# Optimization experiments

Measured on AMD Instinct MI355X. Metric: run time of the kernel, lower is better.

Reference implementation:

```python
import jax, jax.numpy as jnp
import numpy as np

DN = ('NCHW', 'OIHW', 'NCHW')
BN_EPS = 1e-5


def _conv3x3(x, w, b):
    y = jax.lax.conv_general_dilated(x, w, (1, 1), ((1, 1), (1, 1)), dimension_numbers=DN)
    return y + b[None, :, None, None]


def _bn(x, g, b, m, v):
    # eval-mode BatchNorm with running stats
    scale = g * jax.lax.rsqrt(v + BN_EPS)
    return (x - m[None, :, None, None]) * scale[None, :, None, None] + b[None, :, None, None]


def _bilinear_gather(x, py, px):
    # x: [B,C,H,W]; py, px: [B,K,H,W] float sampling coords (zero padding outside)
    B, C, H, W = x.shape
    y0 = jnp.floor(py)
    x0 = jnp.floor(px)
    wy = py - y0
    wx = px - x0
    y0i = y0.astype(jnp.int32)
    x0i = x0.astype(jnp.int32)
    xf = x.reshape(B, C, H * W)

    def corner(yi, xi, wgt):
        valid = (yi >= 0) & (yi < H) & (xi >= 0) & (xi < W)
        idx = jnp.clip(yi, 0, H - 1) * W + jnp.clip(xi, 0, W - 1)  # [B,K,H,W]
        g = jax.vmap(lambda xb, ib: xb[:, ib])(xf, idx)            # [B,C,K,H,W]
        return g * (wgt * valid.astype(x.dtype))[:, None]

    v = corner(y0i, x0i, (1 - wy) * (1 - wx))
    v = v + corner(y0i, x0i + 1, (1 - wy) * wx)
    v = v + corner(y0i + 1, x0i, wy * (1 - wx))
    v = v + corner(y0i + 1, x0i + 1, wy * wx)
    return v  # [B,C,K,H,W]


def _deform_conv(x, offset, mask, w):
    # modulated deformable conv: 3x3, stride 1, pad 1, dilation 1, groups=1, dg=1
    B, C, H, W = x.shape
    K = 9
    ky = jnp.arange(K) // 3 - 1  # kernel row offsets
    kx = jnp.arange(K) % 3 - 1   # kernel col offsets
    dy = offset[:, :K]           # [B,K,H,W]
    dx = offset[:, K:]
    py = dy + (ky[:, None, None] + jnp.arange(H)[None, :, None]).astype(x.dtype)
    px = dx + (kx[:, None, None] + jnp.arange(W)[None, None, :]).astype(x.dtype)
    val = _bilinear_gather(x, py, px) * mask[:, None]  # [B,C,K,H,W]
    O = w.shape[0]
    return jnp.einsum('bckhw,ock->bohw', val, w.reshape(O, C, K))


def _deconv(x, w):
    # ConvTranspose2d k=4 s=2 p=1, bias=False; torch weight layout [Cin, Cout, 4, 4]
    wk = jnp.flip(w, (2, 3)).transpose(1, 0, 2, 3)  # [Cout, Cin, 4, 4]
    return jax.lax.conv_general_dilated(x, wk, (1, 1), ((2, 2), (2, 2)),
                                        lhs_dilation=(2, 2), dimension_numbers=DN)


def setup_inputs() -> dict:
    key = jax.random.key(0)
    ks = jax.random.split(key, 14)
    B, Cin, Cout, H, W = 8, 256, 256, 64, 64
    x = jax.random.normal(ks[0], (B, Cin, H, W), jnp.float32)
    w_off = jax.random.normal(ks[1], (27, Cin, 3, 3), jnp.float32) * 0.01
    b_off = jnp.zeros((27,), jnp.float32)
    w_dcn = jax.random.normal(ks[2], (Cout, Cin, 3, 3), jnp.float32) * (2.0 / (Cin * 9)) ** 0.5
    gamma1 = 1.0 + 0.1 * jax.random.normal(ks[3], (Cout,), jnp.float32)
    beta1 = 0.1 * jax.random.normal(ks[4], (Cout,), jnp.float32)
    mean1 = 0.1 * jax.random.normal(ks[5], (Cout,), jnp.float32)
    var1 = jax.random.uniform(ks[6], (Cout,), jnp.float32, 0.5, 1.5)
    w_up = jax.random.normal(ks[7], (Cout, Cout, 4, 4), jnp.float32) * 0.05
    gamma2 = 1.0 + 0.1 * jax.random.normal(ks[8], (Cout,), jnp.float32)
    beta2 = 0.1 * jax.random.normal(ks[9], (Cout,), jnp.float32)
    mean2 = 0.1 * jax.random.normal(ks[10], (Cout,), jnp.float32)
    var2 = jax.random.uniform(ks[11], (Cout,), jnp.float32, 0.5, 1.5)
    return dict(x=x, w_off=w_off, b_off=b_off, w_dcn=w_dcn,
                gamma1=gamma1, beta1=beta1, mean1=mean1, var1=var1,
                w_up=w_up, gamma2=gamma2, beta2=beta2, mean2=mean2, var2=var2)


def reference(x, w_off, b_off, w_dcn, gamma1, beta1, mean1, var1,
              w_up, gamma2, beta2, mean2, var2):
    offset_mask = _conv3x3(x, w_off, b_off)          # [B,27,H,W]
    ox, oy, m = jnp.split(offset_mask, 3, axis=1)
    offset = jnp.concatenate([ox, oy], axis=1)       # [B,18,H,W]
    mask = jax.nn.sigmoid(m)                         # [B,9,H,W]
    y = _deform_conv(x, offset, mask, w_dcn)
    y = jax.nn.relu(_bn(y, gamma1, beta1, mean1, var1))
    up = _deconv(y, w_up)
    up = jax.nn.relu(_bn(up, gamma2, beta2, mean2, var2))
    return (y, up)
```

## Files before the change

kernel.cpp:

```cpp
#include <hip/hip_runtime.h>
#include <cstddef>


#define B_EPS 1e-5f

typedef __bf16 bf16x8 __attribute__((ext_vector_type(8)));
typedef float f32x4 __attribute__((ext_vector_type(4)));
typedef unsigned short u16;
typedef unsigned int u32;

__device__ __forceinline__ u32 bfr(float f) {
    u32 u = __float_as_uint(f);
    return (u + 0x7FFFu + ((u >> 16) & 1u)) >> 16;
}

__device__ __forceinline__ void gather8(const float* cb2, uint4 q, int g8, f32x4* ga) {
    const float* p00 = cb2 + ((size_t)(q.x & 0xFFFFu) << 5) + g8;
    const float* p01 = cb2 + ((size_t)(q.x >> 16) << 5) + g8;
    const float* p10 = cb2 + ((size_t)(q.y & 0xFFFFu) << 5) + g8;
    const float* p11 = cb2 + ((size_t)(q.y >> 16) << 5) + g8;
    ga[0] = *(const f32x4*)p00; ga[1] = *(const f32x4*)(p00 + 4);
    ga[2] = *(const f32x4*)p01; ga[3] = *(const f32x4*)(p01 + 4);
    ga[4] = *(const f32x4*)p10; ga[5] = *(const f32x4*)(p10 + 4);
    ga[6] = *(const f32x4*)p11; ga[7] = *(const f32x4*)(p11 + 4);
}

__device__ __forceinline__ uint4 packv(uint4 q, const f32x4* ga) {
    const float w00 = __uint_as_float(q.z << 16);
    const float w01 = __uint_as_float(q.z & 0xFFFF0000u);
    const float w10 = __uint_as_float(q.w << 16);
    const float w11 = __uint_as_float(q.w & 0xFFFF0000u);
    union { bf16x8 h; uint4 u; } r;
#pragma unroll
    for (int jj = 0; jj < 4; ++jj) {
        r.h[jj]     = (__bf16)fmaf(w00, ga[0][jj], fmaf(w01, ga[2][jj], fmaf(w10, ga[4][jj], w11 * ga[6][jj])));
        r.h[4 + jj] = (__bf16)fmaf(w00, ga[1][jj], fmaf(w01, ga[3][jj], fmaf(w10, ga[5][jj], w11 * ga[7][jj])));
    }
    return r.u;
}

__global__ __launch_bounds__(256) void k_tr_woff(const float* __restrict__ w,
                                                 float* __restrict__ o) {
    int i = blockIdx.x * 256 + threadIdx.x;
    int t9 = i % 9; int r = i / 9; int c = r & 255; int co = r >> 8;
    o[c * 243 + co * 9 + t9] = w[i];
}

__global__ __launch_bounds__(256) void k_prep_wdb(const float* __restrict__ w,
                                                  u16* __restrict__ o) {
    int i = blockIdx.x * 256 + threadIdx.x;
    int kk = i & 31; int e = i >> 5;
    int oc = e & 255; int ch = e >> 8;
    int cc = ch & 7; int k = ch >> 3;
    o[i] = (u16)bfr(w[oc * 2304 + (cc * 32 + kk) * 9 + k]);
}

__global__ __launch_bounds__(256) void k_prep_wtb(const float* __restrict__ w,
                                                  u16* __restrict__ o) {
    int i = blockIdx.x * 256 + threadIdx.x;
    int kk = i & 31; int e = i >> 5;
    int oc = e & 255; e >>= 8;
    int cc = e & 31; int cls = e >> 5;
    int tap = kk >> 3, ci = cc * 8 + (kk & 7);
    int ca = cls >> 1, cb = cls & 1;
    int wr = (tap >> 1) ? (ca ? 0 : 1) : (ca ? 2 : 3);
    int wc = (tap & 1) ? (cb ? 0 : 1) : (cb ? 2 : 3);
    o[i] = (u16)bfr(w[ci * 4096 + oc * 16 + wr * 4 + wc]);
}

__global__ __launch_bounds__(256) void k_bn_prep(
    const float* g1, const float* be1, const float* mu1, const float* va1,
    const float* g2, const float* be2, const float* mu2, const float* va2,
    float* bnp) {
    int t = threadIdx.x;
    float s1 = g1[t] * rsqrtf(va1[t] + B_EPS);
    bnp[t] = s1; bnp[256 + t] = be1[t] - mu1[t] * s1;
    float s2 = g2[t] * rsqrtf(va2[t] + B_EPS);
    bnp[512 + t] = s2; bnp[768 + t] = be2[t] - mu2[t] * s2;
}

__global__ __launch_bounds__(256) void k_om_init(const float* __restrict__ b_off,
                                                 float* __restrict__ om) {
    int i = blockIdx.x * 256 + threadIdx.x;
    int co = (i >> 12) % 27;
    om[i] = b_off[co];
}

__global__ __launch_bounds__(256) void k_tr_x(const float* __restrict__ x,
                                              float* __restrict__ xt) {
    const int t = threadIdx.x;
    const int pg = blockIdx.x & 15;
    const int cc = (blockIdx.x >> 4) & 7;
    const int b = blockIdx.x >> 7;
    const int pix = (pg << 8) + t;
    const float* xp = x + ((size_t)b << 20) + ((size_t)(cc << 5) << 12) + pix;
    float v[32];
#pragma unroll
    for (int cl = 0; cl < 32; ++cl) v[cl] = xp[(size_t)cl << 12];
    float* op = xt + ((size_t)b << 20) + ((size_t)cc << 17) + ((size_t)pix << 5);
#pragma unroll
    for (int i = 0; i < 8; ++i)
        *(f32x4*)(op + i * 4) = *(const f32x4*)&v[i * 4];
}

__global__ __launch_bounds__(256) void k_tr_y(const float* __restrict__ y,
                                              u16* __restrict__ yt) {
    const int t = threadIdx.x;
    const int blk = blockIdx.x % 18;
    const int oc = (blockIdx.x / 18) & 7;
    const int b = blockIdx.x / 144;
    const int hp = blk * 256 + t;
    if (hp >= 4356) return;
    const int h = hp / 66, w = hp % 66;
    u16* dstb = yt + (((size_t)b * 32 + oc * 4) * 4356 + hp) * 8;
    if (h == 0 || h == 65 || w == 0 || w == 65) {
        uint4 z = make_uint4(0, 0, 0, 0);
#pragma unroll
        for (int j = 0; j < 4; ++j)
            *(uint4*)(dstb + (size_t)j * (4356 * 8)) = z;
        return;
    }
    const float* yp = y + ((size_t)b << 20) + ((size_t)(oc * 32) << 12)
                    + ((h - 1) << 6) + (w - 1);
    u16 vv[32];
#pragma unroll
    for (int cl = 0; cl < 32; ++cl) vv[cl] = (u16)bfr(yp[(size_t)cl << 12]);
#pragma unroll
    for (int j = 0; j < 4; ++j)
        *(uint4*)(dstb + (size_t)j * (4356 * 8)) = *(const uint4*)&vv[j * 8];
}

__global__ __launch_bounds__(256) void k_offset_conv_part(
    const float* __restrict__ x, const float* __restrict__ wofft,
    float* __restrict__ om)
{
    const int t = threadIdx.x;
    const int chunk = blockIdx.x & 7;
    const int rg = (blockIdx.x >> 3) & 15;
    const int b = blockIdx.x >> 7;
    const int h = (rg << 2) + (t >> 6);
    const int w = t & 63;
    const int c0 = chunk << 5;
    const float* xb = x + ((size_t)b << 20);
    float acc[27];
#pragma unroll
    for (int i = 0; i < 27; ++i) acc[i] = 0.f;
    for (int cl = 0; cl < 32; ++cl) {
        const int c = c0 + cl;
        const float* xc = xb + (c << 12);
        float xv[9];
#pragma unroll
        for (int tr = 0; tr < 3; ++tr) {
            int hh = h + tr - 1;
            bool vy = (unsigned)hh < 64u;
#pragma unroll
            for (int tc = 0; tc < 3; ++tc) {
                int ww = w + tc - 1;
                xv[tr * 3 + tc] = (vy && (unsigned)ww < 64u) ? xc[(hh << 6) + ww] : 0.f;
            }
        }
        const float* wc = wofft + c * 243;
#pragma unroll
        for (int co = 0; co < 27; ++co)
#pragma unroll
            for (int k = 0; k < 9; ++k)
                acc[co] = fmaf(xv[k], wc[co * 9 + k], acc[co]);
    }
    float* omb = om + (size_t)b * 110592 + (h << 6) + w;
#pragma unroll
    for (int co = 0; co < 27; ++co)
        atomicAdd(&omb[co << 12], acc[co]);
}

__global__ __launch_bounds__(256) void k_prep_coeff(
    const float* __restrict__ om, uint4* __restrict__ cpk)
{
    int i = blockIdx.x * 256 + threadIdx.x;
    int pix = i & 4095;
    int bk = i >> 12;
    int k = bk % 9;
    int b = bk / 9;
    int h = pix >> 6, w = pix & 63;
    const float* omb = om + (size_t)b * 110592;
    float dy = omb[(k << 12) + pix];
    float dx = omb[((9 + k) << 12) + pix];
    float mr = omb[((18 + k) << 12) + pix];
    float m  = 1.f / (1.f + __expf(-mr));
    float py = dy + (float)(k / 3 - 1 + h);
    float px = dx + (float)(k % 3 - 1 + w);
    float y0f = floorf(py), x0f = floorf(px);
    float wy = py - y0f, wx = px - x0f;
    int y0 = (int)y0f, x0 = (int)x0f;
    int y1 = y0 + 1, x1 = x0 + 1;
    float vy0 = ((unsigned)y0 < 64u) ? 1.f : 0.f;
    float vy1 = ((unsigned)y1 < 64u) ? 1.f : 0.f;
    float vx0 = ((unsigned)x0 < 64u) ? 1.f : 0.f;
    float vx1 = ((unsigned)x1 < 64u) ? 1.f : 0.f;
    int cy0 = min(max(y0, 0), 63), cy1 = min(max(y1, 0), 63);
    int cx0 = min(max(x0, 0), 63), cx1 = min(max(x1, 0), 63);
    u32 xw = (u32)((cy0 << 6) + cx0) | ((u32)((cy0 << 6) + cx1) << 16);
    u32 yw = (u32)((cy1 << 6) + cx0) | ((u32)((cy1 << 6) + cx1) << 16);
    float w00 = m * (1.f - wy) * (1.f - wx) * vy0 * vx0;
    float w01 = m * (1.f - wy) * wx         * vy0 * vx1;
    float w10 = m * wy         * (1.f - wx) * vy1 * vx0;
    float w11 = m * wy         * wx         * vy1 * vx1;
    u32 zw = bfr(w00) | (bfr(w01) << 16);
    u32 ww2 = bfr(w10) | (bfr(w11) << 16);
    cpk[i] = make_uint4(xw, yw, zw, ww2);
}

__global__ __launch_bounds__(256, 2) void k_deform_mfma(
    const float* __restrict__ xt, const u16* __restrict__ Wdb,
    const uint4* __restrict__ cpk, const float* __restrict__ bnp,
    float* __restrict__ yout)
{
    __shared__ __align__(16) u16 sB[2][64 * 40];
    const int t = threadIdx.x;
    const int row = blockIdx.x & 63;
    const int b = blockIdx.x >> 6;
    const int pix0 = row << 6;
    const int p = t >> 2;
    const int g = t & 3;
    const int g8 = g << 3;
    const float* xtb = xt + ((size_t)b << 20);

    const int lane = t & 63;
    const int wv = t >> 6;
    const int quad = lane >> 4;
    const int ln = lane & 15;
    const u16* Wrow = Wdb + (size_t)(wv * 64 + ln) * 32 + quad * 8;

    f32x4 acc[4][4];
#pragma unroll
    for (int i = 0; i < 4; ++i)
#pragma unroll
        for (int j = 0; j < 4; ++j) acc[i][j] = (f32x4)0.f;

    bf16x8 afb[2][4];
    uint4 qcur = cpk[(size_t)(b * 9) * 4096 + pix0 + p];
    {
#pragma unroll
        for (int mi = 0; mi < 4; ++mi)
            afb[0][mi] = *(const bf16x8*)(Wrow + mi * 512);
        f32x4 ga[8];
        gather8(xtb, qcur, g8, ga);
        *(uint4*)&sB[0][p * 40 + g8] = packv(qcur, ga);
        __syncthreads();
    }

    for (int k = 0; k < 9; ++k) {
        uint4 qnext = qcur;
        if (k < 8) qnext = cpk[(size_t)(b * 9 + k + 1) * 4096 + pix0 + p];
#pragma unroll
        for (int cc = 0; cc < 8; ++cc) {
            const int ch = k * 8 + cc;
            const int par = cc & 1;
            const bool pre = ch < 71;
            const uint4 q = (cc == 7) ? qnext : qcur;
            f32x4 ga[8];
            if (pre) {
                const u16* Wn = Wrow + (size_t)(ch + 1) * 8192;
#pragma unroll
                for (int mi = 0; mi < 4; ++mi)
                    afb[par ^ 1][mi] = *(const bf16x8*)(Wn + mi * 512);
                gather8(xtb + ((size_t)((cc + 1) & 7) << 17), q, g8, ga);
            }
            bf16x8 bg[4];
#pragma unroll
            for (int i = 0; i < 4; ++i)
                bg[i] = *(const bf16x8*)&sB[par][(i * 16 + ln) * 40 + quad * 8];
#pragma unroll
            for (int mi = 0; mi < 4; ++mi)
#pragma unroll
                for (int ni = 0; ni < 4; ++ni)
                    acc[mi][ni] = __builtin_amdgcn_mfma_f32_16x16x32_bf16(
                        afb[par][mi], bg[ni], acc[mi][ni], 0, 0, 0);
            if (pre)
                *(uint4*)&sB[par ^ 1][p * 40 + g8] = packv(q, ga);
            __syncthreads();
        }
        qcur = qnext;
    }

    const float* sc1 = bnp;
    const float* bi1 = bnp + 256;
    float* yb2 = yout + ((size_t)b << 20);
#pragma unroll
    for (int mi = 0; mi < 4; ++mi) {
#pragma unroll
        for (int r = 0; r < 4; ++r) {
            int o = wv * 64 + mi * 16 + quad * 4 + r;
            float sc = sc1[o], bi = bi1[o];
#pragma unroll
            for (int ni = 0; ni < 4; ++ni) {
                float v = fmaxf(fmaf(acc[mi][ni][r], sc, bi), 0.f);
                yb2[((size_t)o << 12) + pix0 + ni * 16 + ln] = v;
            }
        }
    }
}

__global__ __launch_bounds__(256, 4) void k_deconv_mfma(
    const u16* __restrict__ yt, const u16* __restrict__ Wtb,
    const float* __restrict__ bnp, float* __restrict__ up)
{
    const int t = threadIdx.x;
    const int h0 = blockIdx.x & 63;
    const int cls = (blockIdx.x >> 6) & 3;
    const int b = blockIdx.x >> 8;
    const int ca = cls >> 1, cb = cls & 1;
    const int DH0 = ca ? 0 : -1, DH1 = ca ? 1 : 0;
    const int DW0 = cb ? 0 : -1, DW1 = cb ? 1 : 0;

    const int lane = t & 63;
    const int wv = t >> 6;
    const int quad = lane >> 4;
    const int ln = lane & 15;

    const int DHq = (quad >> 1) ? DH1 : DH0;
    const int DWq = (quad & 1) ? DW1 : DW0;

    const u16* ytb = yt + (size_t)b * (32u * 4356 * 8);
    const u16* Bb[4];
#pragma unroll
    for (int i = 0; i < 4; ++i) {
        int pix = i * 16 + ln;
        Bb[i] = ytb + (size_t)((h0 + DHq + 1) * 66 + (pix + DWq + 1)) * 8;
    }
    const u16* Ab = Wtb + (size_t)(cls * 32) * 8192
                  + (size_t)(wv * 64 + ln) * 32 + quad * 8;

    f32x4 acc[4][4];
#pragma unroll
    for (int i = 0; i < 4; ++i)
#pragma unroll
        for (int j = 0; j < 4; ++j) acc[i][j] = (f32x4)0.f;

#pragma unroll 2
    for (int cc = 0; cc < 32; ++cc) {
        bf16x8 af[4], bg[4];
#pragma unroll
        for (int mi = 0; mi < 4; ++mi)
            af[mi] = *(const bf16x8*)(Ab + (size_t)cc * 8192 + mi * 512);
#pragma unroll
        for (int i = 0; i < 4; ++i)
            bg[i] = *(const bf16x8*)(Bb[i] + (size_t)cc * (4356 * 8));
#pragma unroll
        for (int mi = 0; mi < 4; ++mi)
#pragma unroll
            for (int ni = 0; ni < 4; ++ni)
                acc[mi][ni] = __builtin_amdgcn_mfma_f32_16x16x32_bf16(
                    af[mi], bg[ni], acc[mi][ni], 0, 0, 0);
    }

    const float* sc2 = bnp + 512;
    const float* bi2 = bnp + 768;
    float* ub = up + ((size_t)b << 22);
    const int pr = (h0 << 1) + ca;
#pragma unroll
    for (int mi = 0; mi < 4; ++mi) {
#pragma unroll
        for (int r = 0; r < 4; ++r) {
            int o = wv * 64 + mi * 16 + quad * 4 + r;
            float sc = sc2[o], bi = bi2[o];
#pragma unroll
            for (int ni = 0; ni < 4; ++ni) {
                int qc = ((ni * 16 + ln) << 1) + cb;
                float v = fmaxf(fmaf(acc[mi][ni][r], sc, bi), 0.f);
                ub[((size_t)o << 14) + (pr << 7) + qc] = v;
            }
        }
    }
}

extern "C" void kernel_launch(void* const* d_in, const int* in_sizes, int n_in,
                              void* d_out, int out_size, void* d_ws, size_t ws_size,
                              hipStream_t stream)
{
    const float* x     = (const float*)d_in[0];
    const float* w_off = (const float*)d_in[1];
    const float* b_off = (const float*)d_in[2];
    const float* w_dcn = (const float*)d_in[3];
    const float* g1    = (const float*)d_in[4];
    const float* be1   = (const float*)d_in[5];
    const float* mu1   = (const float*)d_in[6];
    const float* va1   = (const float*)d_in[7];
    const float* w_up  = (const float*)d_in[8];
    const float* g2    = (const float*)d_in[9];
    const float* be2   = (const float*)d_in[10];
    const float* mu2   = (const float*)d_in[11];
    const float* va2   = (const float*)d_in[12];

    float* yout = (float*)d_out;
    float* up   = (float*)d_out + 8388608;
    float* xt   = up;

    char* ws = (char*)d_ws;
    float* om    = (float*)(ws + 0);
    float* wofft = (float*)(ws + 3538944);
    uint4* cpk   = (uint4*)(ws + 3787776);
    u16*   Wdb   = (u16*)  (ws + 8506368);
    u16*   yt    = (u16*)  (ws + 0);
    u16*   Wtb   = (u16*)  (ws + 17842176);
    float* bnp   = (float*)(ws + 19939328);

    k_tr_woff   <<<243,  256, 0, stream>>>(w_off, wofft);
    k_prep_wdb  <<<2304, 256, 0, stream>>>(w_dcn, Wdb);
    k_prep_wtb  <<<4096, 256, 0, stream>>>(w_up, Wtb);
    k_bn_prep   <<<1,    256, 0, stream>>>(g1, be1, mu1, va1, g2, be2, mu2, va2, bnp);
    k_om_init   <<<3456, 256, 0, stream>>>(b_off, om);
    k_tr_x      <<<1024, 256, 0, stream>>>(x, xt);
    k_offset_conv_part<<<1024, 256, 0, stream>>>(x, wofft, om);
    k_prep_coeff<<<1152, 256, 0, stream>>>(om, cpk);
    k_deform_mfma<<<512, 256, 0, stream>>>(xt, Wdb, cpk, bnp, yout);
    k_tr_y      <<<1152, 256, 0, stream>>>(yout, yt);
    k_deconv_mfma<<<2048,256, 0, stream>>>(yt, Wtb, bnp, up);
}
```

Baseline: 561.1 us.

## Compute offset conv with split-bf16 MFMA implicit GEMM instead of scalar FMA

Replaces the scalar FP32 offset/mask 3x3 convolution, which used per-chunk atomicAdd partial sums, with an MFMA implicit GEMM. Input and weights are split into bf16 hi and lo parts, and three MFMA products per tile approximate FP32 accuracy. The input is pre-transposed into a padded channel-blocked layout. Per-wave partial sums are reduced in shared memory and written once with the bias folded in, which removes the om init kernel and the atomics. It adds a new prep kernel plus extra scratch traffic, and uses space in the output buffer as scratch.

```diff
diff --git a/kernel.cpp b/kernel.cpp
--- a/kernel.cpp
+++ b/kernel.cpp
@@ -37,13 +37,6 @@
         r.h[4 + jj] = (__bf16)fmaf(w00, ga[1][jj], fmaf(w01, ga[3][jj], fmaf(w10, ga[5][jj], w11 * ga[7][jj])));
     }
     return r.u;
-}
-
-__global__ __launch_bounds__(256) void k_tr_woff(const float* __restrict__ w,
-                                                 float* __restrict__ o) {
-    int i = blockIdx.x * 256 + threadIdx.x;
-    int t9 = i % 9; int r = i / 9; int c = r & 255; int co = r >> 8;
-    o[c * 243 + co * 9 + t9] = w[i];
 }
 
 __global__ __launch_bounds__(256) void k_prep_wdb(const float* __restrict__ w,
@@ -68,6 +61,22 @@
     o[i] = (u16)bfr(w[ci * 4096 + oc * 16 + wr * 4 + wc]);
 }
 
+__global__ __launch_bounds__(256) void k_prep_wob(const float* __restrict__ w,
+                                                  u16* __restrict__ o) {
+    int i = blockIdx.x * 256 + threadIdx.x;
+    int kk = i & 31; int e = i >> 5;
+    int oc = e & 31; e >>= 5;
+    int part = e & 1; int ch = e >> 1;
+    int cc = ch & 7, k = ch >> 3;
+    float v = (oc < 27) ? w[oc * 2304 + (cc * 32 + kk) * 9 + k] : 0.f;
+    u16 hh = bfr(v);
+    if (part) {
+        float vh = __uint_as_float((u32)hh << 16);
+        hh = (u16)bfr(v - vh);
+    }
+    o[i] = hh;
+}
+
 __global__ __launch_bounds__(256) void k_bn_prep(
     const float* g1, const float* be1, const float* mu1, const float* va1,
     const float* g2, const float* be2, const float* mu2, const float* va2,
@@ -79,13 +88,6 @@
     bnp[512 + t] = s2; bnp[768 + t] = be2[t] - mu2[t] * s2;
 }
 
-__global__ __launch_bounds__(256) void k_om_init(const float* __restrict__ b_off,
-                                                 float* __restrict__ om) {
-    int i = blockIdx.x * 256 + threadIdx.x;
-    int co = (i >> 12) % 27;
-    om[i] = b_off[co];
-}
-
 __global__ __launch_bounds__(256) void k_tr_x(const float* __restrict__ x,
                                               float* __restrict__ xt) {
     const int t = threadIdx.x;
@@ -101,6 +103,44 @@
 #pragma unroll
     for (int i = 0; i < 8; ++i)
         *(f32x4*)(op + i * 4) = *(const f32x4*)&v[i * 4];
+}
+
+__global__ __launch_bounds__(256) void k_prep_xth(const float* __restrict__ x,
+                                                  u16* __restrict__ xo) {
+    const int t = threadIdx.x;
+    const int blk = blockIdx.x % 18;
+    const int ccg = (blockIdx.x / 18) & 7;
+    const int b = blockIdx.x / 144;
+    const int hp = blk * 256 + t;
+    if (hp >= 4356) return;
+    const int h = hp / 66, w = hp % 66;
+    const size_t PL = 4356u * 8u;
+    u16* dh = xo + ((size_t)b * 64 + ccg * 4) * PL + (size_t)hp * 8;
+    u16* dl = dh + 32 * PL;
+    if (h == 0 || h == 65 || w == 0 || w == 65) {
+        uint4 z = make_uint4(0, 0, 0, 0);
+#pragma unroll
+        for (int j = 0; j < 4; ++j) {
+            *(uint4*)(dh + (size_t)j * PL) = z;
+            *(uint4*)(dl + (size_t)j * PL) = z;
+        }
+        return;
+    }
+    const float* xp = x + ((size_t)b << 20) + ((size_t)(ccg * 32) << 12)
+                    + ((h - 1) << 6) + (w - 1);
+    u16 vh[32], vl[32];
+#pragma unroll
+    for (int cl = 0; cl < 32; ++cl) {
+        float v = xp[(size_t)cl << 12];
+        u16 hh = (u16)bfr(v);
+        vh[cl] = hh;
+        vl[cl] = (u16)bfr(v - __uint_as_float((u32)hh << 16));
+    }
+#pragma unroll
+    for (int j = 0; j < 4; ++j) {
+        *(uint4*)(dh + (size_t)j * PL) = *(const uint4*)&vh[j * 8];
+        *(uint4*)(dl + (size_t)j * PL) = *(const uint4*)&vl[j * 8];
+    }
 }
 
 __global__ __launch_bounds__(256) void k_tr_y(const float* __restrict__ y,
@@ -130,46 +170,81 @@
         *(uint4*)(dstb + (size_t)j * (4356 * 8)) = *(const uint4*)&vv[j * 8];
 }
 
-__global__ __launch_bounds__(256) void k_offset_conv_part(
-    const float* __restrict__ x, const float* __restrict__ wofft,
-    float* __restrict__ om)
+__global__ __launch_bounds__(256, 2) void k_offset_mfma(
+    const u16* __restrict__ xth, const u16* __restrict__ Wob,
+    const float* __restrict__ b_off, float* __restrict__ om)
 {
-    const int t = threadIdx.x;
-    const int chunk = blockIdx.x & 7;
-    const int rg = (blockIdx.x >> 3) & 15;
-    const int b = blockIdx.x >> 7;
-    const int h = (rg << 2) + (t >> 6);
-    const int w = t & 63;
-    const int c0 = chunk << 5;
-    const float* xb = x + ((size_t)b << 20);
-    float acc[27];
-#pragma unroll
-    for (int i = 0; i < 27; ++i) acc[i] = 0.f;
-    for (int cl = 0; cl < 32; ++cl) {
-        const int c = c0 + cl;
-        const float* xc = xb + (c << 12);
-        float xv[9];
-#pragma unroll
-        for (int tr = 0; tr < 3; ++tr) {
-            int hh = h + tr - 1;
-            bool vy = (unsigned)hh < 64u;
-#pragma unroll
-            for (int tc = 0; tc < 3; ++tc) {
-                int ww = w + tc - 1;
-                xv[tr * 3 + tc] = (vy && (unsigned)ww < 64u) ? xc[(hh << 6) + ww] : 0.f;
+    __shared__ float sR[4][2048];
+    const int t = threadIdx.x;
+    const int h0 = blockIdx.x & 63;
+    const int b = blockIdx.x >> 6;
+    const int wv = t >> 6;
+    const int lane = t & 63;
+    const int quad = lane >> 4;
+    const int ln = lane & 15;
+    const size_t PL = 4356u * 8u;
+    const u16* xbb = xth + (size_t)b * 64 * PL;
+
+    f32x4 acc[2][4];
+#pragma unroll
+    for (int i = 0; i < 2; ++i)
+#pragma unroll
+        for (int j = 0; j < 4; ++j) acc[i][j] = (f32x4)0.f;
+
+#pragma unroll 3
+    for (int ci = 0; ci < 18; ++ci) {
+        const int ch = wv * 18 + ci;
+        const int k = ch >> 3, cc = ch & 7;
+        const int dy = k / 3, dx = k - dy * 3;
+        const int hp = (h0 + dy) * 66 + dx + ln;
+        const u16* Bh = xbb + (size_t)((cc << 2) + quad) * PL + (size_t)hp * 8;
+        const u16* Bl = Bh + 32 * PL;
+        const u16* Ap = Wob + ch * 2048 + ln * 32 + (quad << 3);
+        bf16x8 ah[2], al[2], bh[4], bl[4];
+        ah[0] = *(const bf16x8*)(Ap);
+        ah[1] = *(const bf16x8*)(Ap + 512);
+        al[0] = *(const bf16x8*)(Ap + 1024);
+        al[1] = *(const bf16x8*)(Ap + 1536);
+#pragma unroll
+        for (int ni = 0; ni < 4; ++ni) {
+            bh[ni] = *(const bf16x8*)(Bh + ni * 128);
+            bl[ni] = *(const bf16x8*)(Bl + ni * 128);
+        }
+#pragma unroll
+        for (int mi = 0; mi < 2; ++mi)
+#pragma unroll
+            for (int ni = 0; ni < 4; ++ni) {
+                acc[mi][ni] = __builtin_amdgcn_mfma_f32_16x16x32_bf16(
+                    ah[mi], bh[ni], acc[mi][ni], 0, 0, 0);
+                acc[mi][ni] = __builtin_amdgcn_mfma_f32_16x16x32_bf16(
+                    al[mi], bh[ni], acc[mi][ni], 0, 0, 0);
+                acc[mi][ni] = __builtin_amdgcn_mfma_f32_16x16x32_bf16(
+                    ah[mi], bl[ni], acc[mi][ni], 0, 0, 0);
             }
-        }
-        const float* wc = wofft + c * 243;
-#pragma unroll
-        for (int co = 0; co < 27; ++co)
-#pragma unroll
-            for (int k = 0; k < 9; ++k)
-                acc[co] = fmaf(xv[k], wc[co * 9 + k], acc[co]);
-    }
-    float* omb = om + (size_t)b * 110592 + (h << 6) + w;
-#pragma unroll
-    for (int co = 0; co < 27; ++co)
-        atomicAdd(&omb[co << 12], acc[co]);
+    }
+
+    float* sw = &sR[wv][0];
+#pragma unroll
+    for (int mi = 0; mi < 2; ++mi)
+#pragma unroll
+        for (int ni = 0; ni < 4; ++ni)
+            *(f32x4*)&sw[((mi << 2) + ni) * 256 + (lane << 2)] = acc[mi][ni];
+    __syncthreads();
+
+#pragma unroll
+    for (int j = 0; j < 8; ++j) {
+        int flat = (t << 3) + j;
+        int e = flat >> 8;
+        int rem = flat & 255;
+        int l2 = rem >> 2, r = rem & 3;
+        int co = ((e >> 2) << 4) + ((l2 >> 4) << 2) + r;
+        if (co < 27) {
+            float s = sR[0][flat] + sR[1][flat] + sR[2][flat] + sR[3][flat];
+            int w = ((e & 3) << 4) + (l2 & 15);
+            om[(size_t)b * 110592 + ((size_t)co << 12) + (h0 << 6) + w]
+                = s + b_off[co];
+        }
+    }
 }
 
 __global__ __launch_bounds__(256) void k_prep_coeff(
@@ -394,23 +469,24 @@
     float* yout = (float*)d_out;
     float* up   = (float*)d_out + 8388608;
     float* xt   = up;
+    u16*   xth  = (u16*)((char*)up + 33554432);
 
     char* ws = (char*)d_ws;
     float* om    = (float*)(ws + 0);
-    float* wofft = (float*)(ws + 3538944);
     uint4* cpk   = (uint4*)(ws + 3787776);
+    u16*   Wob   = (u16*)  (ws + 3787776);
     u16*   Wdb   = (u16*)  (ws + 8506368);
     u16*   yt    = (u16*)  (ws + 0);
     u16*   Wtb   = (u16*)  (ws + 17842176);
     float* bnp   = (float*)(ws + 19939328);
 
-    k_tr_woff   <<<243,  256, 0, stream>>>(w_off, wofft);
     k_prep_wdb  <<<2304, 256, 0, stream>>>(w_dcn, Wdb);
     k_prep_wtb  <<<4096, 256, 0, stream>>>(w_up, Wtb);
+    k_prep_wob  <<<576,  256, 0, stream>>>(w_off, Wob);
     k_bn_prep   <<<1,    256, 0, stream>>>(g1, be1, mu1, va1, g2, be2, mu2, va2, bnp);
-    k_om_init   <<<3456, 256, 0, stream>>>(b_off, om);
     k_tr_x      <<<1024, 256, 0, stream>>>(x, xt);
-    k_offset_conv_part<<<1024, 256, 0, stream>>>(x, wofft, om);
+    k_prep_xth  <<<1152, 256, 0, stream>>>(x, xth);
+    k_offset_mfma<<<512, 256, 0, stream>>>(xth, Wob, b_off, om);
     k_prep_coeff<<<1152, 256, 0, stream>>>(om, cpk);
     k_deform_mfma<<<512, 256, 0, stream>>>(xt, Wdb, cpk, bnp, yout);
     k_tr_y      <<<1152, 256, 0, stream>>>(yout, yt);
```

New measurement: 492.6 us. 1.14x faster.
